# Optimization experiments

Measured on AMD Instinct MI355X. Metric: run time of the kernel, lower is better.

## Reference

```python
import jax, jax.numpy as jnp
import numpy as np

B, H, W, DIM = 8, 32, 32, 768
HEADS = 12
HD = DIM // HEADS  # 64


def setup_inputs() -> dict:
    key = jax.random.key(0)
    ks = jax.random.split(key, 7)
    s = 0.02  # init scale to keep logits in a sane range
    return {
        "x": jax.random.normal(ks[0], (B, H, W, DIM), jnp.float32),
        "qkv_w": jax.random.normal(ks[1], (3 * DIM, DIM), jnp.float32) * s,
        "qkv_b": jax.random.normal(ks[2], (3 * DIM,), jnp.float32) * s,
        "proj_w": jax.random.normal(ks[3], (DIM, DIM), jnp.float32) * s,
        "proj_b": jax.random.normal(ks[4], (DIM,), jnp.float32) * s,
        "rel_pos_h": jax.random.normal(ks[5], (2 * H - 1, HD), jnp.float32) * s,
        "rel_pos_w": jax.random.normal(ks[6], (2 * W - 1, HD), jnp.float32) * s,
    }


def reference(x, qkv_w, qkv_b, proj_w, proj_b, rel_pos_h, rel_pos_w):
    b, h, w, dim = x.shape
    n = h * w
    hd = dim // HEADS
    scale = hd ** -0.5

    xf = x.reshape(b, n, dim)
    qkv = xf @ qkv_w.T + qkv_b                       # (B, N, 3*dim)
    qkv = qkv.reshape(b, n, 3, HEADS, hd)
    qkv = jnp.transpose(qkv, (2, 0, 3, 1, 4)).reshape(3, b * HEADS, n, hd)
    q, k, v = qkv[0], qkv[1], qkv[2]                 # each (B*heads, N, hd)

    # decomposed rel-pos bias (q_size == k_size -> pure index lookup)
    coords_h = jnp.arange(h)[:, None] - jnp.arange(h)[None, :] + (h - 1)
    coords_w = jnp.arange(w)[:, None] - jnp.arange(w)[None, :] + (w - 1)
    Rh = rel_pos_h[coords_h]                         # (H, H, hd)
    Rw = rel_pos_w[coords_w]                         # (W, W, hd)
    r_q = q.reshape(b * HEADS, h, w, hd)
    rel_h = jnp.einsum('bhwc,hkc->bhwk', r_q, Rh)    # (B*heads, H, W, H)
    rel_w = jnp.einsum('bhwc,wkc->bhwk', r_q, Rw)    # (B*heads, H, W, W)
    bias = (rel_h[:, :, :, :, None] + rel_w[:, :, :, None, :]).reshape(b * HEADS, n, n)

    attn = (q * scale) @ jnp.swapaxes(k, -2, -1) + bias
    attn = jax.nn.softmax(attn, axis=-1)
    out = attn @ v                                   # (B*heads, N, hd)

    out = out.reshape(b, HEADS, n, hd)
    out = jnp.transpose(out, (0, 2, 1, 3)).reshape(b, n, dim)
    out = out @ proj_w.T + proj_b
    return out.reshape(b, h, w, dim)
```

## Files before the change

### kernel.cpp

```cpp
#include <hip/hip_runtime.h>
#include <hip/hip_bf16.h>

typedef unsigned short u16;
typedef __attribute__((ext_vector_type(8))) short bf16x8;
typedef __attribute__((ext_vector_type(4))) short s16x4;
typedef __attribute__((ext_vector_type(4))) float f32x4;

#define QSCALE 0.18033688011116012f
#define RPSCALE 8.0f
#define EXP2(x) __builtin_amdgcn_exp2f(x)

__device__ __forceinline__ float bf2f(u16 u) {
  union { unsigned int i; float f; } v; v.i = ((unsigned int)u) << 16; return v.f;
}
__device__ __forceinline__ u16 f2bf(float f) {
  union { float f; unsigned int i; } v; v.f = f;
  unsigned int r = v.i + 0x7fffu + ((v.i >> 16) & 1u);
  return (u16)(r >> 16);
}
__device__ __forceinline__ unsigned int pk2bf(float a, float b) {
  union { __hip_bfloat162 h; unsigned int u; } cv;
  cv.h = __float22bfloat162_rn(float2{a, b});
  return cv.u;
}
__device__ __forceinline__ f32x4 MFMA(bf16x8 a, bf16x8 b, f32x4 c) {
  return __builtin_amdgcn_mfma_f32_16x16x32_bf16(a, b, c, 0, 0, 0);
}
__device__ __forceinline__ void cvt8(const float* p, uint4* dst) {
  float4 f0 = *(const float4*)(p);
  float4 f1 = *(const float4*)(p + 4);
  u16* t = (u16*)dst;
  t[0] = f2bf(f0.x); t[1] = f2bf(f0.y); t[2] = f2bf(f0.z); t[3] = f2bf(f0.w);
  t[4] = f2bf(f1.x); t[5] = f2bf(f1.y); t[6] = f2bf(f1.z); t[7] = f2bf(f1.w);
}
__device__ __forceinline__ void cvt8s(const float* p, uint4* dst, float s) {
  float4 f0 = *(const float4*)(p);
  float4 f1 = *(const float4*)(p + 4);
  u16* t = (u16*)dst;
  t[0] = f2bf(f0.x * s); t[1] = f2bf(f0.y * s); t[2] = f2bf(f0.z * s); t[3] = f2bf(f0.w * s);
  t[4] = f2bf(f1.x * s); t[5] = f2bf(f1.y * s); t[6] = f2bf(f1.z * s); t[7] = f2bf(f1.w * s);
}
__device__ __forceinline__ void gld16(const u16* g, u16* l) {
  __builtin_amdgcn_global_load_lds(
      (const __attribute__((address_space(1))) unsigned int*)g,
      (__attribute__((address_space(3))) unsigned int*)l, 16, 0, 0);
}

#define N8_X  786432
#define N8_QW 221184
#define N8_PW 73728
__global__ __launch_bounds__(256) void cast_kernel(
    const float* __restrict__ x, const float* __restrict__ qw, const float* __restrict__ pw,
    u16* __restrict__ xb, u16* __restrict__ qwb, u16* __restrict__ pwb)
{
  const int i = blockIdx.x * 256 + threadIdx.x;
  const float* s; u16* d; int off;
  if (i < N8_X)            { s = x;  d = xb;  off = i; }
  else if (i < N8_X+N8_QW) { s = qw; d = qwb; off = i - N8_X; }
  else                     { s = pw; d = pwb; off = i - (N8_X + N8_QW); }
  uint4 pk; cvt8(s + (size_t)off * 8, &pk);
  *(uint4*)(d + (size_t)off * 8) = pk;
}

template<int MODE, int NXB>
__global__ __launch_bounds__(256) void gemm_bt(
    const u16* __restrict__ A, const u16* __restrict__ Bw, const float* __restrict__ bias,
    void* __restrict__ C0v, u16* __restrict__ C1, u16* __restrict__ C2,
    int M, int N, int K)
{
  __shared__ u16 sA[128 * 32];
  __shared__ u16 sB[128 * 32];
  const int tid = threadIdx.x;
  const int lane = tid & 63, wv = tid >> 6;
  const int wr = wv >> 1, wc = wv & 1;
  const int l16 = lane & 15, quad = lane >> 4;
  const int bi = blockIdx.x;
  const int t = bi >> 3;
  const int nx = t % NXB;
  const int my = ((t / NXB) << 3) | (bi & 7);
  const int m0 = my << 7, n0 = nx << 7;

  const int srow = tid >> 2, scol = (tid & 3) << 3;
  const u16* gA0 = A  + (size_t)(m0 + srow) * K + scol;
  const u16* gB0 = Bw + (size_t)(n0 + srow) * K + scol;
  const u16* gA1 = gA0 + (size_t)64 * K;
  const u16* gB1 = gB0 + (size_t)64 * K;
  u16* const lwA0 = sA + wv * 512;
  u16* const lwA1 = sA + 2048 + wv * 512;
  u16* const lwB0 = sB + wv * 512;
  u16* const lwB1 = sB + 2048 + wv * 512;

  f32x4 acc[4][4];
  #pragma unroll
  for (int i = 0; i < 4; ++i)
    #pragma unroll
    for (int j = 0; j < 4; ++j) {
      acc[i][j][0] = 0.f; acc[i][j][1] = 0.f; acc[i][j][2] = 0.f; acc[i][j][3] = 0.f;
    }

  for (int k0 = 0; k0 < K; k0 += 32) {
    __syncthreads();
    gld16(gA0 + k0, lwA0);
    gld16(gA1 + k0, lwA1);
    gld16(gB0 + k0, lwB0);
    gld16(gB1 + k0, lwB1);
    __syncthreads();
    bf16x8 af[4], bfr[4];
    #pragma unroll
    for (int i = 0; i < 4; ++i)
      af[i] = *(const bf16x8*)(sA + (wr * 64 + i * 16 + l16) * 32 + quad * 8);
    #pragma unroll
    for (int j = 0; j < 4; ++j)
      bfr[j] = *(const bf16x8*)(sB + (wc * 64 + j * 16 + l16) * 32 + quad * 8);
    #pragma unroll
    for (int i = 0; i < 4; ++i)
      #pragma unroll
      for (int j = 0; j < 4; ++j)
        acc[i][j] = MFMA(af[i], bfr[j], acc[i][j]);
  }

  #pragma unroll
  for (int j = 0; j < 4; ++j) {
    const int n = n0 + wc * 64 + j * 16 + l16;
    const float bv = bias[n];
    if (MODE == 0) {
      float* C0 = (float*)C0v;
      #pragma unroll
      for (int i = 0; i < 4; ++i) {
        const int m = m0 + wr * 64 + i * 16 + quad * 4;
        #pragma unroll
        for (int r = 0; r < 4; ++r)
          C0[(size_t)(m + r) * N + n] = acc[i][j][r] + bv;
      }
    } else {
      u16* C0 = (u16*)C0v;
      const int which = n / 768;
      const int rem = n - which * 768;
      const int head = rem >> 6, c = rem & 63;
      #pragma unroll
      for (int i = 0; i < 4; ++i) {
        const int m = m0 + wr * 64 + i * 16 + quad * 4;
        const int b = m >> 10, npos = m & 1023;
        const size_t bh = (size_t)(b * 12 + head);
        if (which == 0) {
          #pragma unroll
          for (int r = 0; r < 4; ++r)
            C0[(bh << 16) + ((size_t)(npos + r) << 6) + c] =
                f2bf((acc[i][j][r] + bv) * QSCALE);
        } else if (which == 1) {
          const size_t base = ((bh * 16 + (size_t)(npos >> 6)) << 12)
                            + (size_t)((((npos >> 4) & 3) * 2 + (c >> 5)) << 9)
                            + (size_t)((((npos & 15) + 16 * ((c >> 3) & 3)) << 3) + (c & 7));
          #pragma unroll
          for (int r = 0; r < 4; ++r)
            C1[base + r * 8] = f2bf(acc[i][j][r] + bv);
        } else {
          const size_t base = ((bh * 16 + (size_t)(npos >> 6)) << 12)
                            + (size_t)(((((npos >> 5) & 1) * 4 + (c >> 4))) << 9)
                            + (size_t)((((c & 15) + 16 * ((npos >> 3) & 3)) << 3) + (npos & 7));
          s16x4 pk;
          #pragma unroll
          for (int r = 0; r < 4; ++r) pk[r] = (short)f2bf(acc[i][j][r] + bv);
          *(s16x4*)(C2 + base) = pk;
        }
      }
    }
  }
}

__global__ __launch_bounds__(256) void attn_kernel(
    const u16* __restrict__ Q, const u16* __restrict__ Kf, const u16* __restrict__ Vf,
    const float* __restrict__ rph, const float* __restrict__ rpw,
    u16* __restrict__ Oa)
{
  __shared__ __align__(16) u16 uni[9216];
  __shared__ u16 sSh[4 * 16 * 36];

  u16* const uRPH = uni;
  u16* const uRPW = uni + 4536;

  const int tid = threadIdx.x;
  const int wave = tid >> 6, lane = tid & 63;
  const int l16 = lane & 15, quad = lane >> 4;
  const int bi = blockIdx.x;
  const int t = bi >> 3;
  const int qb = t & 15;
  const int bh = ((t >> 4) << 3) | (bi & 7);
  const int qrow0 = (qb << 6) + (wave << 4);
  const int qh = qrow0 >> 5;
  const int qwb = qrow0 & 31;

  u16* const pw = uni + wave * 1152;
  u16* const sShw = sSh + wave * 576;

  bf16x8 qf[2];
  {
    const u16* qp = Q + (((size_t)bh << 10) + qrow0 + l16) * 64 + quad * 8;
    qf[0] = *(const bf16x8*)(qp);
    qf[1] = *(const bf16x8*)(qp + 32);
  }

  for (int j = tid; j < 64 * 8; j += 256) {
    const int row = j >> 3, ck = (j & 7) << 3;
    uint4 vw;
    if (row < 63) cvt8s(rpw + (size_t)row * 64 + ck, &vw, RPSCALE);
    else { vw.x = 0u; vw.y = 0u; vw.z = 0u; vw.w = 0u; }
    *(uint4*)(uRPW + row * 72 + ck) = vw;
    if (row < 63) {
      uint4 vh;
      cvt8s(rph + (size_t)row * 64 + ck, &vh, RPSCALE);
      *(uint4*)(uRPH + row * 72 + ck) = vh;
    }
  }
  __syncthreads();

  #pragma unroll
  for (int tk = 0; tk < 2; ++tk) {
    const int kh = tk * 16 + l16;
    const u16* bp = uRPH + (qh + 31 - kh) * 72 + quad * 8;
    bf16x8 b0 = *(const bf16x8*)(bp);
    bf16x8 b1 = *(const bf16x8*)(bp + 32);
    f32x4 c; c[0] = 0.f; c[1] = 0.f; c[2] = 0.f; c[3] = 0.f;
    c = MFMA(qf[0], b0, c);
    c = MFMA(qf[1], b1, c);
    #pragma unroll
    for (int r = 0; r < 4; ++r)
      sShw[(quad * 4 + r) * 36 + tk * 16 + l16] = f2bf(c[r]);
  }

  f32x4 swc[4];
  #pragma unroll
  for (int tj = 0; tj < 4; ++tj) {
    const u16* bp = uRPW + (tj * 16 + l16) * 72 + quad * 8;
    bf16x8 b0 = *(const bf16x8*)(bp);
    bf16x8 b1 = *(const bf16x8*)(bp + 32);
    f32x4 c; c[0] = 0.f; c[1] = 0.f; c[2] = 0.f; c[3] = 0.f;
    c = MFMA(qf[0], b0, c);
    c = MFMA(qf[1], b1, c);
    swc[tj] = c;
  }
  __syncthreads();

  #pragma unroll
  for (int tj = 0; tj < 4; ++tj)
    #pragma unroll
    for (int r = 0; r < 4; ++r)
      pw[(quad * 4 + r) * 72 + tj * 16 + l16] = f2bf(swc[tj][r]);

  float rw[2][4];
  #pragma unroll
  for (int hi = 0; hi < 2; ++hi)
    #pragma unroll
    for (int r = 0; r < 4; ++r) {
      const int kw = hi * 16 + quad * 4 + r;
      rw[hi][r] = bf2f(pw[l16 * 72 + (qwb + l16 - kw + 31)]);
    }

  f32x4 oacc[4];
  #pragma unroll
  for (int nd = 0; nd < 4; ++nd) {
    oacc[nd][0] = 0.f; oacc[nd][1] = 0.f; oacc[nd][2] = 0.f; oacc[nd][3] = 0.f;
  }
  float lsum = 0.f;

  const u16* const Kfb = Kf + (((size_t)bh) << 16) + lane * 8;
  const u16* const Vfb = Vf + (((size_t)bh) << 16) + lane * 8;

  for (int kt = 0; kt < 16; ++kt) {
    const u16* Kp = Kfb + ((size_t)kt << 12);
    const u16* Vp = Vfb + ((size_t)kt << 12);
    float rh[2];
    {
      const unsigned int w2 =
          *(const unsigned int*)(sShw + l16 * 36 + (kt << 1));
      rh[0] = bf2f((u16)(w2 & 0xffffu));
      rh[1] = bf2f((u16)(w2 >> 16));
    }
    f32x4 sacc[4];
    #pragma unroll
    for (int mk = 0; mk < 4; ++mk) {
      bf16x8 kf0 = *(const bf16x8*)(Kp + ((mk * 2 + 0) << 9));
      bf16x8 kf1 = *(const bf16x8*)(Kp + ((mk * 2 + 1) << 9));
      f32x4 t4; t4[0] = 0.f; t4[1] = 0.f; t4[2] = 0.f; t4[3] = 0.f;
      t4 = MFMA(kf0, qf[0], t4);
      t4 = MFMA(kf1, qf[1], t4);
      sacc[mk] = t4;
    }
    #pragma unroll
    for (int mk = 0; mk < 4; ++mk) {
      const float rhv = rh[mk >> 1];
      const float* rwp = rw[mk & 1];
      float e0 = EXP2(sacc[mk][0] + rhv + rwp[0]);
      float e1 = EXP2(sacc[mk][1] + rhv + rwp[1]);
      float e2 = EXP2(sacc[mk][2] + rhv + rwp[2]);
      float e3 = EXP2(sacc[mk][3] + rhv + rwp[3]);
      lsum += (e0 + e1) + (e2 + e3);
      uint2 pk2; pk2.x = pk2bf(e0, e1); pk2.y = pk2bf(e2, e3);
      *(uint2*)(pw + l16 * 72 + mk * 16 + quad * 4) = pk2;
    }
    #pragma unroll
    for (int ks = 0; ks < 2; ++ks) {
      bf16x8 ap = *(const bf16x8*)(pw + l16 * 72 + ks * 32 + quad * 8);
      #pragma unroll
      for (int nd = 0; nd < 4; ++nd) {
        bf16x8 bv = *(const bf16x8*)(Vp + ((ks * 4 + nd) << 9));
        oacc[nd] = MFMA(bv, ap, oacc[nd]);
      }
    }
  }

  lsum += __shfl_xor(lsum, 16);
  lsum += __shfl_xor(lsum, 32);

  const int b = bh / 12, head = bh - b * 12;
  const float linv = 1.0f / lsum;
  const size_t base =
      ((size_t)(b << 10) + qrow0 + l16) * 768 + head * 64 + quad * 4;
  #pragma unroll
  for (int nd = 0; nd < 4; ++nd) {
    s16x4 pk;
    #pragma unroll
    for (int r = 0; r < 4; ++r) pk[r] = (short)f2bf(oacc[nd][r] * linv);
    *(s16x4*)(Oa + base + nd * 16) = pk;
  }
}

extern "C" void kernel_launch(void* const* d_in, const int* in_sizes, int n_in,
                              void* d_out, int out_size, void* d_ws, size_t ws_size,
                              hipStream_t stream) {
  (void)in_sizes; (void)n_in; (void)out_size; (void)ws_size;
  const float* x      = (const float*)d_in[0];
  const float* qkv_w  = (const float*)d_in[1];
  const float* qkv_b  = (const float*)d_in[2];
  const float* proj_w = (const float*)d_in[3];
  const float* proj_b = (const float*)d_in[4];
  const float* rph    = (const float*)d_in[5];
  const float* rpw    = (const float*)d_in[6];
  float* out = (float*)d_out;

  char* ws = (char*)d_ws;
  const size_t SZ = (size_t)96 * 1024 * 64;
  u16* Qw  = (u16*)ws;
  u16* Kfw = Qw + SZ;
  u16* Vfw = Kfw + SZ;
  u16* Xb  = Vfw + SZ;
  u16* Oa  = Xb;
  u16* QWb = Xb + SZ;
  u16* PWb = QWb + (size_t)2304 * 768;

  cast_kernel<<<4224, 256, 0, stream>>>(x, qkv_w, proj_w, Xb, QWb, PWb);
  gemm_bt<1, 18><<<1152, 256, 0, stream>>>(Xb, QWb, qkv_b, Qw, Kfw, Vfw, 8192, 2304, 768);
  attn_kernel<<<1536, 256, 0, stream>>>(Qw, Kfw, Vfw, rph, rpw, Oa);
  gemm_bt<0, 6><<<384, 256, 0, stream>>>(Oa, PWb, proj_b, out, nullptr, nullptr, 8192, 768, 768);
}
```

Before: 222.4 us.

## Halve proj GEMM row tile and double-buffer attention P scratch

Adds a BM template parameter to the GEMM so the output projection runs with 64-row tiles over 768 blocks instead of 384, giving more blocks to fill the GPU's compute units. In the attention kernel, the per-wave P staging buffer alternates between two LDS regions across consecutive key tiles. This is meant to reduce write-after-read hazards and let the compiler overlap the next tile's softmax writes with the previous tile's PV reads. It costs lower MFMA reuse per block in the smaller GEMM and more LDS footprint in attention.

```diff
diff --git a/kernel.cpp b/kernel.cpp
--- a/kernel.cpp
+++ b/kernel.cpp
@@ -62,23 +62,26 @@
   *(uint4*)(d + (size_t)off * 8) = pk;
 }
 
-template<int MODE, int NXB>
+template<int MODE, int NXB, int BM>
 __global__ __launch_bounds__(256) void gemm_bt(
     const u16* __restrict__ A, const u16* __restrict__ Bw, const float* __restrict__ bias,
     void* __restrict__ C0v, u16* __restrict__ C1, u16* __restrict__ C2,
     int M, int N, int K)
 {
-  __shared__ u16 sA[128 * 32];
+  __shared__ u16 sA[BM * 32];
   __shared__ u16 sB[128 * 32];
   const int tid = threadIdx.x;
   const int lane = tid & 63, wv = tid >> 6;
-  const int wr = wv >> 1, wc = wv & 1;
   const int l16 = lane & 15, quad = lane >> 4;
   const int bi = blockIdx.x;
   const int t = bi >> 3;
   const int nx = t % NXB;
   const int my = ((t / NXB) << 3) | (bi & 7);
-  const int m0 = my << 7, n0 = nx << 7;
+  const int m0 = my << (BM == 128 ? 7 : 6), n0 = nx << 7;
+
+  const int rowbase = (BM == 128) ? ((wv >> 1) * 64) : 0;
+  const int colbase = (BM == 128) ? ((wv & 1) * 64) : (wv * 32);
+  const int NJ = (BM == 128) ? 4 : 2;
 
   const int srow = tid >> 2, scol = (tid & 3) << 3;
   const u16* gA0 = A  + (size_t)(m0 + srow) * K + scol;
@@ -86,7 +89,7 @@
   const u16* gA1 = gA0 + (size_t)64 * K;
   const u16* gB1 = gB0 + (size_t)64 * K;
   u16* const lwA0 = sA + wv * 512;
-  u16* const lwA1 = sA + 2048 + wv * 512;
+  u16* const lwA1 = sA + (BM == 128 ? 2048 : 0) + wv * 512;
   u16* const lwB0 = sB + wv * 512;
   u16* const lwB1 = sB + 2048 + wv * 512;
 
@@ -101,33 +104,36 @@
   for (int k0 = 0; k0 < K; k0 += 32) {
     __syncthreads();
     gld16(gA0 + k0, lwA0);
-    gld16(gA1 + k0, lwA1);
+    if (BM == 128) gld16(gA1 + k0, lwA1);
     gld16(gB0 + k0, lwB0);
     gld16(gB1 + k0, lwB1);
     __syncthreads();
     bf16x8 af[4], bfr[4];
     #pragma unroll
     for (int i = 0; i < 4; ++i)
-      af[i] = *(const bf16x8*)(sA + (wr * 64 + i * 16 + l16) * 32 + quad * 8);
+      af[i] = *(const bf16x8*)(sA + (rowbase + i * 16 + l16) * 32 + quad * 8);
     #pragma unroll
     for (int j = 0; j < 4; ++j)
-      bfr[j] = *(const bf16x8*)(sB + (wc * 64 + j * 16 + l16) * 32 + quad * 8);
+      if (j < NJ)
+        bfr[j] = *(const bf16x8*)(sB + (colbase + j * 16 + l16) * 32 + quad * 8);
     #pragma unroll
     for (int i = 0; i < 4; ++i)
       #pragma unroll
       for (int j = 0; j < 4; ++j)
-        acc[i][j] = MFMA(af[i], bfr[j], acc[i][j]);
+        if (j < NJ)
+          acc[i][j] = MFMA(af[i], bfr[j], acc[i][j]);
   }
 
   #pragma unroll
   for (int j = 0; j < 4; ++j) {
-    const int n = n0 + wc * 64 + j * 16 + l16;
+    if (j >= NJ) continue;
+    const int n = n0 + colbase + j * 16 + l16;
     const float bv = bias[n];
     if (MODE == 0) {
       float* C0 = (float*)C0v;
       #pragma unroll
       for (int i = 0; i < 4; ++i) {
-        const int m = m0 + wr * 64 + i * 16 + quad * 4;
+        const int m = m0 + rowbase + i * 16 + quad * 4;
         #pragma unroll
         for (int r = 0; r < 4; ++r)
           C0[(size_t)(m + r) * N + n] = acc[i][j][r] + bv;
@@ -139,7 +145,7 @@
       const int head = rem >> 6, c = rem & 63;
       #pragma unroll
       for (int i = 0; i < 4; ++i) {
-        const int m = m0 + wr * 64 + i * 16 + quad * 4;
+        const int m = m0 + rowbase + i * 16 + quad * 4;
         const int b = m >> 10, npos = m & 1023;
         const size_t bh = (size_t)(b * 12 + head);
         if (which == 0) {
@@ -190,7 +196,8 @@
   const int qh = qrow0 >> 5;
   const int qwb = qrow0 & 31;
 
-  u16* const pw = uni + wave * 1152;
+  u16* const pwA = uni + wave * 1152;
+  u16* const pwB = uni + 4608 + wave * 1152;
   u16* const sShw = sSh + wave * 576;
 
   bf16x8 qf[2];
@@ -245,7 +252,7 @@
   for (int tj = 0; tj < 4; ++tj)
     #pragma unroll
     for (int r = 0; r < 4; ++r)
-      pw[(quad * 4 + r) * 72 + tj * 16 + l16] = f2bf(swc[tj][r]);
+      pwA[(quad * 4 + r) * 72 + tj * 16 + l16] = f2bf(swc[tj][r]);
 
   float rw[2][4];
   #pragma unroll
@@ -253,7 +260,7 @@
     #pragma unroll
     for (int r = 0; r < 4; ++r) {
       const int kw = hi * 16 + quad * 4 + r;
-      rw[hi][r] = bf2f(pw[l16 * 72 + (qwb + l16 - kw + 31)]);
+      rw[hi][r] = bf2f(pwA[l16 * 72 + (qwb + l16 - kw + 31)]);
     }
 
   f32x4 oacc[4];
@@ -266,13 +273,13 @@
   const u16* const Kfb = Kf + (((size_t)bh) << 16) + lane * 8;
   const u16* const Vfb = Vf + (((size_t)bh) << 16) + lane * 8;
 
-  for (int kt = 0; kt < 16; ++kt) {
-    const u16* Kp = Kfb + ((size_t)kt << 12);
-    const u16* Vp = Vfb + ((size_t)kt << 12);
+  auto attn_iter = [&](int ktx, u16* pwb) {
+    const u16* Kp = Kfb + ((size_t)ktx << 12);
+    const u16* Vp = Vfb + ((size_t)ktx << 12);
     float rh[2];
     {
       const unsigned int w2 =
-          *(const unsigned int*)(sShw + l16 * 36 + (kt << 1));
+          *(const unsigned int*)(sShw + l16 * 36 + (ktx << 1));
       rh[0] = bf2f((u16)(w2 & 0xffffu));
       rh[1] = bf2f((u16)(w2 >> 16));
     }
@@ -296,17 +303,22 @@
       float e3 = EXP2(sacc[mk][3] + rhv + rwp[3]);
       lsum += (e0 + e1) + (e2 + e3);
       uint2 pk2; pk2.x = pk2bf(e0, e1); pk2.y = pk2bf(e2, e3);
-      *(uint2*)(pw + l16 * 72 + mk * 16 + quad * 4) = pk2;
+      *(uint2*)(pwb + l16 * 72 + mk * 16 + quad * 4) = pk2;
     }
     #pragma unroll
     for (int ks = 0; ks < 2; ++ks) {
-      bf16x8 ap = *(const bf16x8*)(pw + l16 * 72 + ks * 32 + quad * 8);
+      bf16x8 ap = *(const bf16x8*)(pwb + l16 * 72 + ks * 32 + quad * 8);
       #pragma unroll
       for (int nd = 0; nd < 4; ++nd) {
         bf16x8 bv = *(const bf16x8*)(Vp + ((ks * 4 + nd) << 9));
         oacc[nd] = MFMA(bv, ap, oacc[nd]);
       }
     }
+  };
+
+  for (int kt = 0; kt < 16; kt += 2) {
+    attn_iter(kt, pwA);
+    attn_iter(kt + 1, pwB);
   }
 
   lsum += __shfl_xor(lsum, 16);
@@ -349,7 +361,7 @@
   u16* PWb = QWb + (size_t)2304 * 768;
 
   cast_kernel<<<4224, 256, 0, stream>>>(x, qkv_w, proj_w, Xb, QWb, PWb);
-  gemm_bt<1, 18><<<1152, 256, 0, stream>>>(Xb, QWb, qkv_b, Qw, Kfw, Vfw, 8192, 2304, 768);
+  gemm_bt<1, 18, 128><<<1152, 256, 0, stream>>>(Xb, QWb, qkv_b, Qw, Kfw, Vfw, 8192, 2304, 768);
   attn_kernel<<<1536, 256, 0, stream>>>(Qw, Kfw, Vfw, rph, rpw, Oa);
-  gemm_bt<0, 6><<<384, 256, 0, stream>>>(Oa, PWb, proj_b, out, nullptr, nullptr, 8192, 768, 768);
-}
+  gemm_bt<0, 6, 64><<<768, 256, 0, stream>>>(Oa, PWb, proj_b, out, nullptr, nullptr, 8192, 768, 768);
+}
```

Result: slower. 279.7 us (+25.8%).
